# Kernel tuning notes

Measured on AMD Instinct MI355X. Metric: run time of the kernel, lower is better.

Reference implementation:

```python
import jax, jax.numpy as jnp
import numpy as np

N_NODES = 100000


def gcn_conv(x, src, dst, W, b, n_nodes):
    """PyG-style GCNConv: linear transform, symmetric-normalized aggregation with self loops."""
    h = x @ W  # (N, out)
    e = src.shape[0]
    # degree including the implicit self loop (edge weights = 1)
    deg = jax.ops.segment_sum(jnp.ones((e,), dtype=h.dtype), dst, num_segments=n_nodes) + 1.0
    dis = jax.lax.rsqrt(deg)  # deg^{-1/2}
    coef = dis[src] * dis[dst]  # (E,)
    msg = h[src] * coef[:, None]  # (E, out) -- gather + scale
    agg = jax.ops.segment_sum(msg, dst, num_segments=n_nodes)  # scatter-add
    agg = agg + h * (dis * dis)[:, None]  # self-loop contribution
    return agg + b


def setup_inputs() -> dict:
    key = jax.random.key(0)
    k = jax.random.split(key, 6)
    in_dim, hid, out = 128, 128, 64
    E = 1600000
    x = jax.random.normal(k[0], (N_NODES, in_dim), dtype=jnp.float32)
    edge_index = jax.random.randint(k[1], (2, E), 0, N_NODES, dtype=jnp.int64)
    W1 = jax.random.normal(k[2], (in_dim, hid), dtype=jnp.float32) * (1.0 / np.sqrt(in_dim))
    b1 = jnp.zeros((hid,), dtype=jnp.float32)
    W2 = jax.random.normal(k[3], (hid, out), dtype=jnp.float32) * (1.0 / np.sqrt(hid))
    b2 = jnp.zeros((out,), dtype=jnp.float32)
    return {"x": x, "edge_index": edge_index, "W1": W1, "b1": b1, "W2": W2, "b2": b2}


def reference(x, edge_index, W1, b1, W2, b2):
    src, dst = edge_index[0], edge_index[1]
    h = gcn_conv(x, src, dst, W1, b1, N_NODES)
    h = jax.nn.relu(h)
    # dropout is identity in eval mode
    h = gcn_conv(h, src, dst, W2, b2, N_NODES)
    # L2 normalize along feature dim (F.normalize, eps=1e-12)
    norm = jnp.maximum(jnp.linalg.norm(h, axis=-1, keepdims=True), 1e-12)
    return h / norm
```

## Files before the change

### kernel.cpp

```cpp
#include <hip/hip_runtime.h>
#include <hip/hip_bf16.h>
#include <math.h>

#define CSHIFT 9
#define TILE   4096
#define PSH    14

using f16x8 = __attribute__((ext_vector_type(8))) _Float16;
using f16x2 = __attribute__((ext_vector_type(2))) _Float16;
using f32x4 = __attribute__((ext_vector_type(4))) float;

__device__ __forceinline__ unsigned pack_f16(float lo, float hi) {
    auto h = __builtin_amdgcn_cvt_pkrtz(lo, hi);
    return *(unsigned*)&h;
}
__device__ __forceinline__ f16x2 h2(unsigned u) { return *(f16x2*)&u; }

__device__ __forceinline__ unsigned pack_fp8x4(float f0, float f1, float f2, float f3) {
    int w = 0;
    w = __builtin_amdgcn_cvt_pk_fp8_f32(f0, f1, w, false);
    w = __builtin_amdgcn_cvt_pk_fp8_f32(f2, f3, w, true);
    return (unsigned)w;
}
__device__ __forceinline__ void fp8x4_acc(unsigned v, float& a0, float& a1, float& a2, float& a3) {
    auto lo = __builtin_amdgcn_cvt_pk_f32_fp8((int)v, false);
    auto hi = __builtin_amdgcn_cvt_pk_f32_fp8((int)v, true);
    a0 += lo[0]; a1 += lo[1]; a2 += hi[0]; a3 += hi[1];
}

__global__ void k_prep(const float* __restrict__ W1, const float* __restrict__ W2,
                       unsigned short* __restrict__ wp1, unsigned short* __restrict__ wp2,
                       int* __restrict__ ccursor, int NC) {
    int idx = blockIdx.x * 256 + threadIdx.x;
    if (idx < NC) ccursor[idx] = idx << PSH;
    if (idx < 16384) {
        int e = idx & 7, l = (idx >> 3) & 63, f = idx >> 9;
        int nt = f & 7, kt = f >> 3;
        int k = kt * 32 + (l >> 4) * 8 + e, nn = nt * 16 + (l & 15);
        _Float16 hv = (_Float16)W1[k * 128 + nn];
        wp1[idx] = *(unsigned short*)&hv;
    }
    int i2 = idx - 16384;
    if (i2 >= 0 && i2 < 8192) {
        int e = i2 & 7, l = (i2 >> 3) & 63, f = i2 >> 9;
        int nt = f & 3, kt = f >> 2;
        int k = kt * 32 + (l >> 4) * 8 + e, nn = nt * 16 + (l & 15);
        _Float16 hv = (_Float16)W2[k * 64 + nn];
        wp2[i2] = *(unsigned short*)&hv;
    }
}

__global__ __launch_bounds__(256) void k_part(const int* __restrict__ src,
                                              const int* __restrict__ dst, int E,
                                              int* __restrict__ ccursor,
                                              int* __restrict__ pairs, int NC) {
    __shared__ int sdst[TILE];
    __shared__ int stg[TILE];
    __shared__ unsigned char sbk[TILE];
    __shared__ int h[256], delta[256], cur[256];
    __shared__ int sa[256], sb[256];
    int t = threadIdx.x;
    int base = blockIdx.x * TILE;
    int cnt = min(TILE, E - base);

    h[t] = 0; __syncthreads();
    #pragma unroll
    for (int k = 0; k < TILE / 256; ++k) {
        int e = base + k * 256 + t;
        int d = (e < E) ? dst[e] : -1;
        sdst[k * 256 + t] = d;
        if (d >= 0) atomicAdd(&h[d >> CSHIFT], 1);
    }
    __syncthreads();
    int myc = h[t];
    int* c_ = sa; int* n_ = sb;
    c_[t] = myc; __syncthreads();
    for (int o = 1; o < 256; o <<= 1) {
        int val = c_[t] + ((t >= o) ? c_[t - o] : 0);
        n_[t] = val; __syncthreads();
        int* tmp = c_; c_ = n_; n_ = tmp;
    }
    int ex = c_[t] - myc;
    cur[t] = ex;
    int g = 0;
    if (t < NC && myc) g = atomicAdd(&ccursor[t], myc);
    delta[t] = g - ex;
    __syncthreads();

    #pragma unroll
    for (int k = 0; k < TILE / 256; ++k) {
        int e = base + k * 256 + t;
        if (e < E) {
            int d = sdst[k * 256 + t];
            int b = d >> CSHIFT;
            int p = atomicAdd(&cur[b], 1);
            stg[p] = src[e] | ((d & 511) << 17);
            sbk[p] = (unsigned char)b;
        }
    }
    __syncthreads();
    for (int i = t; i < cnt; i += 256)
        pairs[delta[sbk[i]] + i] = stg[i];
}

__global__ __launch_bounds__(256) void k_build(const int* __restrict__ ccursor,
                                               const int* __restrict__ pairs,
                                               int2* __restrict__ seg,
                                               float* __restrict__ dis,
                                               int* __restrict__ csr, int N) {
    __shared__ int h[512];
    __shared__ int cur[512];
    __shared__ int sa[256], sb[256];
    int b = blockIdx.x, t = threadIdx.x;
    h[t] = 0; h[t + 256] = 0; __syncthreads();
    int beg = b << PSH, end = ccursor[b];
    for (int i = beg + t; i < end; i += 256) atomicAdd(&h[pairs[i] >> 17], 1);
    __syncthreads();
    int h0 = h[2 * t], h1 = h[2 * t + 1];
    int s = h0 + h1;
    int* c_ = sa; int* n_ = sb;
    c_[t] = s; __syncthreads();
    for (int o = 1; o < 256; o <<= 1) {
        int val = c_[t] + ((t >= o) ? c_[t - o] : 0);
        n_[t] = val; __syncthreads();
        int* tmp = c_; c_ = n_; n_ = tmp;
    }
    int ex = c_[t] - s;
    int d0 = b << CSHIFT;
    int da = d0 + 2 * t, db = da + 1;
    cur[2 * t] = ex; cur[2 * t + 1] = ex + h0;
    if (da < N) { seg[da] = make_int2(beg + ex, beg + ex + h0); dis[da] = rsqrtf((float)h0 + 1.0f); }
    if (db < N) { seg[db] = make_int2(beg + ex + h0, beg + ex + h0 + h1); dis[db] = rsqrtf((float)h1 + 1.0f); }
    __syncthreads();
    for (int i = beg + t; i < end; i += 256) {
        int pk = pairs[i];
        int p = atomicAdd(&cur[pk >> 17], 1);
        csr[beg + p] = pk & 0x1FFFF;
    }
}

__global__ __launch_bounds__(256) void k_gemm1(
    const float* __restrict__ A, const unsigned short* __restrict__ wp,
    const float* __restrict__ dis, unsigned* __restrict__ G, int M)
{
    constexpr int NT = 8;
    constexpr int ND = 32;

    union UW { uint4 q; f16x8 v; };
    union UA { unsigned u[4]; f16x8 v; };

    const int tid  = threadIdx.x;
    const int wv   = tid >> 6;
    const int lane = tid & 63;
    const int lm   = lane & 15;
    const int lk   = lane >> 4;
    const int m0   = blockIdx.x * 128 + wv * 32;

    f16x8 xf[2][4];
    int mrow[2];
    #pragma unroll
    for (int mt = 0; mt < 2; ++mt) {
        int m = m0 + mt * 16 + lm;
        mrow[mt] = m;
        int mc = m < M ? m : (M - 1);
        const float* Ar = A + (size_t)mc * 128;
        #pragma unroll
        for (int kt = 0; kt < 4; ++kt) {
            int cb = kt * 32 + lk * 8;
            float4 p = *(const float4*)(Ar + cb);
            float4 q = *(const float4*)(Ar + cb + 4);
            UA u;
            u.u[0] = pack_f16(p.x, p.y);
            u.u[1] = pack_f16(p.z, p.w);
            u.u[2] = pack_f16(q.x, q.y);
            u.u[3] = pack_f16(q.z, q.w);
            xf[mt][kt] = u.v;
        }
    }

    f32x4 acc[2][NT];
    #pragma unroll
    for (int mt = 0; mt < 2; ++mt)
        #pragma unroll
        for (int nt = 0; nt < NT; ++nt)
            #pragma unroll
            for (int r = 0; r < 4; ++r) acc[mt][nt][r] = 0.f;

    const uint4* wpv = (const uint4*)wp;
    #pragma unroll
    for (int kt = 0; kt < 4; ++kt) {
        f16x8 wf[NT];
        #pragma unroll
        for (int nt = 0; nt < NT; ++nt) {
            UW u; u.q = wpv[(kt * NT + nt) * 64 + lane];
            wf[nt] = u.v;
        }
        #pragma unroll
        for (int mt = 0; mt < 2; ++mt)
            #pragma unroll
            for (int nt = 0; nt < NT; ++nt)
                acc[mt][nt] = __builtin_amdgcn_mfma_f32_16x16x32_f16(
                    wf[nt], xf[mt][kt], acc[mt][nt], 0, 0, 0);
    }

    #pragma unroll
    for (int mt = 0; mt < 2; ++mt) {
        int m = mrow[mt];
        if (m < M) {
            float dd = dis[m];
            unsigned* gr = G + (size_t)m * ND;
            #pragma unroll
            for (int nt = 0; nt < NT; ++nt)
                gr[nt * 4 + lk] = pack_fp8x4(acc[mt][nt][0] * dd, acc[mt][nt][1] * dd,
                                             acc[mt][nt][2] * dd, acc[mt][nt][3] * dd);
        }
    }
}

__global__ __launch_bounds__(256) void k_agg1(
    const unsigned* __restrict__ g1, const int2* __restrict__ seg,
    const int* __restrict__ csr, const float* __restrict__ dis,
    const float* __restrict__ b1, unsigned* __restrict__ y1, int n)
{
    int wid  = (blockIdx.x * 256 + threadIdx.x) >> 6;
    int lane = threadIdx.x & 63;
    if (wid >= n) return;
    int d  = wid;
    int ll = lane & 31;
    int eh = lane >> 5;
    int2 se = seg[d];
    int beg = se.x, end = se.y;

    float a0 = 0.f, a1 = 0.f, a2 = 0.f, a3 = 0.f;
    if (eh == 0)
        fp8x4_acc(g1[(size_t)d * 32 + ll], a0, a1, a2, a3);

    int j = beg;
    for (; j + 16 <= end; j += 16) {
        unsigned v[8];
        #pragma unroll
        for (int k = 0; k < 8; ++k)
            v[k] = g1[(size_t)csr[j + 2 * k + eh] * 32 + ll];
        #pragma unroll
        for (int k = 0; k < 8; ++k)
            fp8x4_acc(v[k], a0, a1, a2, a3);
    }
    if (j + 8 <= end) {
        unsigned v[4];
        #pragma unroll
        for (int k = 0; k < 4; ++k)
            v[k] = g1[(size_t)csr[j + 2 * k + eh] * 32 + ll];
        #pragma unroll
        for (int k = 0; k < 4; ++k)
            fp8x4_acc(v[k], a0, a1, a2, a3);
        j += 8;
    }
    if (j + 4 <= end) {
        unsigned v0 = g1[(size_t)csr[j + eh] * 32 + ll];
        unsigned v1 = g1[(size_t)csr[j + 2 + eh] * 32 + ll];
        fp8x4_acc(v0, a0, a1, a2, a3);
        fp8x4_acc(v1, a0, a1, a2, a3);
        j += 4;
    }
    if (j + 2 <= end) {
        fp8x4_acc(g1[(size_t)csr[j + eh] * 32 + ll], a0, a1, a2, a3);
        j += 2;
    }
    if (eh == 0 && j < end)
        fp8x4_acc(g1[(size_t)csr[j] * 32 + ll], a0, a1, a2, a3);

    a0 += __shfl_xor(a0, 32, 64);
    a1 += __shfl_xor(a1, 32, 64);
    a2 += __shfl_xor(a2, 32, 64);
    a3 += __shfl_xor(a3, 32, 64);

    float dd = dis[d];
    float4 bb = *(const float4*)(b1 + 4 * ll);
    float o0 = fmaxf(fmaf(dd, a0, bb.x), 0.f);
    float o1 = fmaxf(fmaf(dd, a1, bb.y), 0.f);
    float o2 = fmaxf(fmaf(dd, a2, bb.z), 0.f);
    float o3 = fmaxf(fmaf(dd, a3, bb.w), 0.f);
    if (lane < 32) {
        uint2 w;
        w.x = pack_f16(o0, o1);
        w.y = pack_f16(o2, o3);
        *((uint2*)(y1 + (size_t)d * 64) + ll) = w;
    }
}

__global__ __launch_bounds__(256) void k_gemm2(
    const unsigned short* __restrict__ A, const unsigned short* __restrict__ wp,
    const float* __restrict__ dis, unsigned* __restrict__ G, int M)
{
    constexpr int NT = 4;
    constexpr int ND = 32;
    union UW { uint4 q; f16x8 v; };

    const int tid  = threadIdx.x;
    const int wv   = tid >> 6;
    const int lane = tid & 63;
    const int lm   = lane & 15;
    const int lk   = lane >> 4;
    const int m0   = blockIdx.x * 128 + wv * 32;

    f16x8 xf[2][4];
    int mrow[2];
    #pragma unroll
    for (int mt = 0; mt < 2; ++mt) {
        int m = m0 + mt * 16 + lm;
        mrow[mt] = m;
        int mc = m < M ? m : (M - 1);
        const uint4* Ar = (const uint4*)(A + (size_t)mc * 128);
        #pragma unroll
        for (int kt = 0; kt < 4; ++kt) {
            UW u; u.q = Ar[kt * 4 + lk];
            xf[mt][kt] = u.v;
        }
    }

    f32x4 acc[2][NT];
    #pragma unroll
    for (int mt = 0; mt < 2; ++mt)
        #pragma unroll
        for (int nt = 0; nt < NT; ++nt)
            #pragma unroll
            for (int r = 0; r < 4; ++r) acc[mt][nt][r] = 0.f;

    const uint4* wpv = (const uint4*)wp;
    #pragma unroll
    for (int kt = 0; kt < 4; ++kt) {
        f16x8 wf[NT];
        #pragma unroll
        for (int nt = 0; nt < NT; ++nt) {
            UW u; u.q = wpv[(kt * NT + nt) * 64 + lane];
            wf[nt] = u.v;
        }
        #pragma unroll
        for (int mt = 0; mt < 2; ++mt)
            #pragma unroll
            for (int nt = 0; nt < NT; ++nt)
                acc[mt][nt] = __builtin_amdgcn_mfma_f32_16x16x32_f16(
                    wf[nt], xf[mt][kt], acc[mt][nt], 0, 0, 0);
    }

    #pragma unroll
    for (int mt = 0; mt < 2; ++mt) {
        int m = mrow[mt];
        if (m < M) {
            float dd = dis[m];
            unsigned* gr = G + (size_t)m * ND;
            #pragma unroll
            for (int nt = 0; nt < NT; ++nt) {
                uint2 w;
                w.x = pack_f16(acc[mt][nt][0] * dd, acc[mt][nt][1] * dd);
                w.y = pack_f16(acc[mt][nt][2] * dd, acc[mt][nt][3] * dd);
                *(uint2*)(gr + nt * 8 + lk * 2) = w;
            }
        }
    }
}

__global__ __launch_bounds__(256) void k_agg2(
    const unsigned* __restrict__ g2, const int2* __restrict__ seg,
    const int* __restrict__ csr, const float* __restrict__ dis,
    const float* __restrict__ b2, float* __restrict__ out, int n)
{
    int wid  = (blockIdx.x * 256 + threadIdx.x) >> 6;
    int lane = threadIdx.x & 63;
    if (wid >= n) return;
    int d  = wid;
    int ql = lane & 15;
    int qh = lane >> 4;
    int2 se = seg[d];
    int beg = se.x, end = se.y;

    f16x2 cx0 = {0, 0}, cx1 = {0, 0}, cy0 = {0, 0}, cy1 = {0, 0};
    int j = beg;
    for (; j + 32 <= end; j += 32) {
        uint2 v[8];
        #pragma unroll
        for (int k = 0; k < 8; ++k) {
            int s = csr[j + 4 * k + qh];
            v[k] = *((const uint2*)(g2 + (size_t)s * 32) + ql);
        }
        #pragma unroll
        for (int k = 0; k < 8; k += 2) {
            cx0 += h2(v[k].x);     cy0 += h2(v[k].y);
            cx1 += h2(v[k + 1].x); cy1 += h2(v[k + 1].y);
        }
    }
    for (; j + 16 <= end; j += 16) {
        int s0 = csr[j      + qh];
        int s1 = csr[j + 4  + qh];
        int s2 = csr[j + 8  + qh];
        int s3 = csr[j + 12 + qh];
        uint2 v0 = *((const uint2*)(g2 + (size_t)s0 * 32) + ql);
        uint2 v1 = *((const uint2*)(g2 + (size_t)s1 * 32) + ql);
        uint2 v2 = *((const uint2*)(g2 + (size_t)s2 * 32) + ql);
        uint2 v3 = *((const uint2*)(g2 + (size_t)s3 * 32) + ql);
        cx0 += h2(v0.x); cy0 += h2(v0.y);
        cx1 += h2(v1.x); cy1 += h2(v1.y);
        cx0 += h2(v2.x); cy0 += h2(v2.y);
        cx1 += h2(v3.x); cy1 += h2(v3.y);
    }
    if (j + 8 <= end) {
        int s0 = csr[j     + qh];
        int s1 = csr[j + 4 + qh];
        uint2 v0 = *((const uint2*)(g2 + (size_t)s0 * 32) + ql);
        uint2 v1 = *((const uint2*)(g2 + (size_t)s1 * 32) + ql);
        cx0 += h2(v0.x); cy0 += h2(v0.y);
        cx1 += h2(v1.x); cy1 += h2(v1.y);
        j += 8;
    }
    for (; j < end; j += 4) {
        if (j + qh < end) {
            int s = csr[j + qh];
            uint2 v = *((const uint2*)(g2 + (size_t)s * 32) + ql);
            cx0 += h2(v.x); cy0 += h2(v.y);
        }
    }
    f16x2 mx = cx0 + cx1;
    f16x2 my = cy0 + cy1;
    float a0 = (float)mx[0], a1 = (float)mx[1];
    float a2 = (float)my[0], a3 = (float)my[1];

    a0 += __shfl_xor(a0, 16, 64); a0 += __shfl_xor(a0, 32, 64);
    a1 += __shfl_xor(a1, 16, 64); a1 += __shfl_xor(a1, 32, 64);
    a2 += __shfl_xor(a2, 16, 64); a2 += __shfl_xor(a2, 32, 64);
    a3 += __shfl_xor(a3, 16, 64); a3 += __shfl_xor(a3, 32, 64);

    uint2 sv = *((const uint2*)(g2 + (size_t)d * 32) + ql);
    f16x2 sx = h2(sv.x), sy = h2(sv.y);
    a0 += (float)sx[0]; a1 += (float)sx[1];
    a2 += (float)sy[0]; a3 += (float)sy[1];

    float dd = dis[d];
    float4 bb = *(const float4*)(b2 + 4 * ql);
    float v0 = fmaf(dd, a0, bb.x);
    float v1 = fmaf(dd, a1, bb.y);
    float v2 = fmaf(dd, a2, bb.z);
    float v3 = fmaf(dd, a3, bb.w);

    float ss = v0 * v0 + v1 * v1 + v2 * v2 + v3 * v3;
    #pragma unroll
    for (int o = 8; o >= 1; o >>= 1)
        ss += __shfl_xor(ss, o, 64);
    float inv = 1.0f / fmaxf(sqrtf(ss), 1e-12f);
    if (lane < 16) {
        float4 w = make_float4(v0 * inv, v1 * inv, v2 * inv, v3 * inv);
        *((float4*)(out + (size_t)d * 64) + ql) = w;
    }
}

extern "C" void kernel_launch(void* const* d_in, const int* in_sizes, int n_in,
                              void* d_out, int out_size, void* d_ws, size_t ws_size,
                              hipStream_t stream) {
    const float* x  = (const float*)d_in[0];
    const int*   ei = (const int*)d_in[1];
    const float* W1 = (const float*)d_in[2];
    const float* b1 = (const float*)d_in[3];
    const float* W2 = (const float*)d_in[4];
    const float* b2 = (const float*)d_in[5];

    const int N = in_sizes[0] / 128;
    const int E = in_sizes[1] / 2;
    const int* src = ei;
    const int* dst = ei + E;
    const int NC = (N + 511) >> CSHIFT;
    const int PB = (E + TILE - 1) / TILE;

    char* ws = (char*)d_ws;
    size_t cur = 0;
    auto alloc = [&](size_t bytes) -> void* {
        void* p = ws + cur;
        cur += (bytes + 255) & ~(size_t)255;
        return p;
    };
    int2*           seg     = (int2*)           alloc((size_t)N * 8);
    int*            ccursor = (int*)            alloc((size_t)NC * 4);
    float*          dis     = (float*)          alloc((size_t)N * 4);
    int*            csr     = (int*)            alloc(((size_t)NC << PSH) * 4);
    int*            pairs   = (int*)            alloc(((size_t)NC << PSH) * 4);
    unsigned short* wp1     = (unsigned short*) alloc(16384 * 2);
    unsigned short* wp2     = (unsigned short*) alloc(8192 * 2);
    unsigned*       g1      = (unsigned*)       alloc((size_t)N * 32 * 4);
    unsigned*       y1      = (unsigned*)       alloc((size_t)N * 64 * 4);
    unsigned*       g2      = (unsigned*)       alloc((size_t)N * 32 * 4);
    float*          out     = (float*)d_out;

    k_prep<<<96, 256, 0, stream>>>(W1, W2, wp1, wp2, ccursor, NC);
    k_part<<<PB, 256, 0, stream>>>(src, dst, E, ccursor, pairs, NC);
    k_build<<<NC, 256, 0, stream>>>(ccursor, pairs, seg, dis, csr, N);

    k_gemm1<<<(N + 127) / 128, 256, 0, stream>>>(x, wp1, dis, g1, N);
    k_agg1<<<(N * 64 + 255) / 256, 256, 0, stream>>>(g1, seg, csr, dis, b1, y1, N);
    k_gemm2<<<(N + 127) / 128, 256, 0, stream>>>((const unsigned short*)y1, wp2, dis, g2, N);
    k_agg2<<<(N * 64 + 255) / 256, 256, 0, stream>>>(g2, seg, csr, dis, b2, out, N);
}
```

Measured before the change: 178.4 us.

## Compute degrees early, fuse GEMM1 with partitioning, pad CSR segments to 16

Degrees are now counted with global atomics inside the prep kernel, which lets GEMM1 run in the same launch as the edge partitioning instead of waiting for the CSR build. Each node's CSR segment is padded to a multiple of 16 with a dummy index N that points at a zeroed extra row of g1/g2, so the aggregation loops drop their remainder branches. The layer-2 aggregation now accumulates in fp32 instead of fp16. The cost is extra gather traffic for the padding entries and 1.6M global atomics for the degree count.

Result: slower. 221.2 us (+24.0%).

```diff
diff --git a/kernel.cpp b/kernel.cpp
--- a/kernel.cpp
+++ b/kernel.cpp
@@ -5,6 +5,7 @@
 #define CSHIFT 9
 #define TILE   4096
 #define PSH    14
+#define PREPB  96
 
 using f16x8 = __attribute__((ext_vector_type(8))) _Float16;
 using f16x2 = __attribute__((ext_vector_type(2))) _Float16;
@@ -28,11 +29,28 @@
     a0 += lo[0]; a1 += lo[1]; a2 += hi[0]; a3 += hi[1];
 }
 
-__global__ void k_prep(const float* __restrict__ W1, const float* __restrict__ W2,
-                       unsigned short* __restrict__ wp1, unsigned short* __restrict__ wp2,
-                       int* __restrict__ ccursor, int NC) {
+__global__ __launch_bounds__(256) void k_prep(
+    const float* __restrict__ W1, const float* __restrict__ W2,
+    const int* __restrict__ dst, int E,
+    unsigned short* __restrict__ wp1, unsigned short* __restrict__ wp2,
+    int* __restrict__ ccursor, int* __restrict__ deg,
+    unsigned* __restrict__ g1, unsigned* __restrict__ g2, int NC, int N)
+{
+    if ((int)blockIdx.x >= PREPB) {
+        int base = (blockIdx.x - PREPB) * TILE;
+        #pragma unroll
+        for (int k = 0; k < TILE / 256; ++k) {
+            int e = base + k * 256 + threadIdx.x;
+            if (e < E) atomicAdd(&deg[dst[e]], 1);
+        }
+        return;
+    }
     int idx = blockIdx.x * 256 + threadIdx.x;
     if (idx < NC) ccursor[idx] = idx << PSH;
+    if (idx < 32) {
+        g1[(size_t)N * 32 + idx] = 0u;
+        g2[(size_t)N * 32 + idx] = 0u;
+    }
     if (idx < 16384) {
         int e = idx & 7, l = (idx >> 3) & 63, f = idx >> 9;
         int nt = f & 7, kt = f >> 3;
@@ -50,63 +68,136 @@
     }
 }
 
-__global__ __launch_bounds__(256) void k_part(const int* __restrict__ src,
-                                              const int* __restrict__ dst, int E,
-                                              int* __restrict__ ccursor,
-                                              int* __restrict__ pairs, int NC) {
-    __shared__ int sdst[TILE];
-    __shared__ int stg[TILE];
-    __shared__ unsigned char sbk[TILE];
-    __shared__ int h[256], delta[256], cur[256];
-    __shared__ int sa[256], sb[256];
-    int t = threadIdx.x;
-    int base = blockIdx.x * TILE;
-    int cnt = min(TILE, E - base);
-
-    h[t] = 0; __syncthreads();
-    #pragma unroll
-    for (int k = 0; k < TILE / 256; ++k) {
-        int e = base + k * 256 + t;
-        int d = (e < E) ? dst[e] : -1;
-        sdst[k * 256 + t] = d;
-        if (d >= 0) atomicAdd(&h[d >> CSHIFT], 1);
-    }
-    __syncthreads();
-    int myc = h[t];
-    int* c_ = sa; int* n_ = sb;
-    c_[t] = myc; __syncthreads();
-    for (int o = 1; o < 256; o <<= 1) {
-        int val = c_[t] + ((t >= o) ? c_[t - o] : 0);
-        n_[t] = val; __syncthreads();
-        int* tmp = c_; c_ = n_; n_ = tmp;
-    }
-    int ex = c_[t] - myc;
-    cur[t] = ex;
-    int g = 0;
-    if (t < NC && myc) g = atomicAdd(&ccursor[t], myc);
-    delta[t] = g - ex;
-    __syncthreads();
-
-    #pragma unroll
-    for (int k = 0; k < TILE / 256; ++k) {
-        int e = base + k * 256 + t;
-        if (e < E) {
-            int d = sdst[k * 256 + t];
-            int b = d >> CSHIFT;
-            int p = atomicAdd(&cur[b], 1);
-            stg[p] = src[e] | ((d & 511) << 17);
-            sbk[p] = (unsigned char)b;
-        }
-    }
-    __syncthreads();
-    for (int i = t; i < cnt; i += 256)
-        pairs[delta[sbk[i]] + i] = stg[i];
+__global__ __launch_bounds__(256) void k_pg1(
+    const int* __restrict__ src, const int* __restrict__ dst, int E,
+    int* __restrict__ ccursor, int* __restrict__ pairs, int NC, int PB,
+    const float* __restrict__ x, const unsigned short* __restrict__ wp1,
+    const int* __restrict__ deg, unsigned* __restrict__ g1, int M)
+{
+    if ((int)blockIdx.x < PB) {
+        __shared__ int stg[TILE];
+        __shared__ unsigned char sbk[TILE];
+        __shared__ int h[256], delta[256], cur[256];
+        __shared__ int sa[256], sb[256];
+        int t = threadIdx.x;
+        int base = blockIdx.x * TILE;
+        int cnt = min(TILE, E - base);
+
+        h[t] = 0; __syncthreads();
+        #pragma unroll
+        for (int k = 0; k < TILE / 256; ++k) {
+            int e = base + k * 256 + t;
+            if (e < E) atomicAdd(&h[dst[e] >> CSHIFT], 1);
+        }
+        __syncthreads();
+        int myc = h[t];
+        int* c_ = sa; int* n_ = sb;
+        c_[t] = myc; __syncthreads();
+        for (int o = 1; o < 256; o <<= 1) {
+            int val = c_[t] + ((t >= o) ? c_[t - o] : 0);
+            n_[t] = val; __syncthreads();
+            int* tmp = c_; c_ = n_; n_ = tmp;
+        }
+        int ex = c_[t] - myc;
+        cur[t] = ex;
+        int g = 0;
+        if (t < NC && myc) g = atomicAdd(&ccursor[t], myc);
+        delta[t] = g - ex;
+        __syncthreads();
+
+        #pragma unroll
+        for (int k = 0; k < TILE / 256; ++k) {
+            int e = base + k * 256 + t;
+            if (e < E) {
+                int d = dst[e];
+                int b = d >> CSHIFT;
+                int p = atomicAdd(&cur[b], 1);
+                stg[p] = src[e] | ((d & 511) << 17);
+                sbk[p] = (unsigned char)b;
+            }
+        }
+        __syncthreads();
+        for (int i = t; i < cnt; i += 256)
+            pairs[delta[sbk[i]] + i] = stg[i];
+    } else {
+        constexpr int NT = 8;
+        constexpr int ND = 32;
+        union UW { uint4 q; f16x8 v; };
+        union UA { unsigned u[4]; f16x8 v; };
+
+        const int bid  = blockIdx.x - PB;
+        const int tid  = threadIdx.x;
+        const int wv   = tid >> 6;
+        const int lane = tid & 63;
+        const int lm   = lane & 15;
+        const int lk   = lane >> 4;
+        const int m0   = bid * 128 + wv * 32;
+
+        f16x8 xf[2][4];
+        int mrow[2];
+        #pragma unroll
+        for (int mt = 0; mt < 2; ++mt) {
+            int m = m0 + mt * 16 + lm;
+            mrow[mt] = m;
+            int mc = m < M ? m : (M - 1);
+            const float* Ar = x + (size_t)mc * 128;
+            #pragma unroll
+            for (int kt = 0; kt < 4; ++kt) {
+                int cb = kt * 32 + lk * 8;
+                float4 p = *(const float4*)(Ar + cb);
+                float4 q = *(const float4*)(Ar + cb + 4);
+                UA u;
+                u.u[0] = pack_f16(p.x, p.y);
+                u.u[1] = pack_f16(p.z, p.w);
+                u.u[2] = pack_f16(q.x, q.y);
+                u.u[3] = pack_f16(q.z, q.w);
+                xf[mt][kt] = u.v;
+            }
+        }
+
+        f32x4 acc[2][NT];
+        #pragma unroll
+        for (int mt = 0; mt < 2; ++mt)
+            #pragma unroll
+            for (int nt = 0; nt < NT; ++nt)
+                #pragma unroll
+                for (int r = 0; r < 4; ++r) acc[mt][nt][r] = 0.f;
+
+        const uint4* wpv = (const uint4*)wp1;
+        #pragma unroll
+        for (int kt = 0; kt < 4; ++kt) {
+            f16x8 wf[NT];
+            #pragma unroll
+            for (int nt = 0; nt < NT; ++nt) {
+                UW u; u.q = wpv[(kt * NT + nt) * 64 + lane];
+                wf[nt] = u.v;
+            }
+            #pragma unroll
+            for (int mt = 0; mt < 2; ++mt)
+                #pragma unroll
+                for (int nt = 0; nt < NT; ++nt)
+                    acc[mt][nt] = __builtin_amdgcn_mfma_f32_16x16x32_f16(
+                        wf[nt], xf[mt][kt], acc[mt][nt], 0, 0, 0);
+        }
+
+        #pragma unroll
+        for (int mt = 0; mt < 2; ++mt) {
+            int m = mrow[mt];
+            if (m < M) {
+                float dd = rsqrtf((float)deg[m] + 1.0f);
+                unsigned* gr = g1 + (size_t)m * ND;
+                #pragma unroll
+                for (int nt = 0; nt < NT; ++nt)
+                    gr[nt * 4 + lk] = pack_fp8x4(acc[mt][nt][0] * dd, acc[mt][nt][1] * dd,
+                                                 acc[mt][nt][2] * dd, acc[mt][nt][3] * dd);
+            }
+        }
+    }
 }
 
 __global__ __launch_bounds__(256) void k_build(const int* __restrict__ ccursor,
                                                const int* __restrict__ pairs,
                                                int2* __restrict__ seg,
-                                               float* __restrict__ dis,
                                                int* __restrict__ csr, int N) {
     __shared__ int h[512];
     __shared__ int cur[512];
@@ -117,7 +208,9 @@
     for (int i = beg + t; i < end; i += 256) atomicAdd(&h[pairs[i] >> 17], 1);
     __syncthreads();
     int h0 = h[2 * t], h1 = h[2 * t + 1];
-    int s = h0 + h1;
+    int p0 = (h0 + 15) & ~15;
+    int p1 = (h1 + 15) & ~15;
+    int s = p0 + p1;
     int* c_ = sa; int* n_ = sb;
     c_[t] = s; __syncthreads();
     for (int o = 1; o < 256; o <<= 1) {
@@ -128,9 +221,11 @@
     int ex = c_[t] - s;
     int d0 = b << CSHIFT;
     int da = d0 + 2 * t, db = da + 1;
-    cur[2 * t] = ex; cur[2 * t + 1] = ex + h0;
-    if (da < N) { seg[da] = make_int2(beg + ex, beg + ex + h0); dis[da] = rsqrtf((float)h0 + 1.0f); }
-    if (db < N) { seg[db] = make_int2(beg + ex + h0, beg + ex + h0 + h1); dis[db] = rsqrtf((float)h1 + 1.0f); }
+    cur[2 * t] = ex; cur[2 * t + 1] = ex + p0;
+    if (da < N) seg[da] = make_int2(beg + ex, beg + ex + p0);
+    if (db < N) seg[db] = make_int2(beg + ex + p0, beg + ex + p0 + p1);
+    for (int i = h0; i < p0; ++i) csr[beg + ex + i] = N;
+    for (int i = h1; i < p1; ++i) csr[beg + ex + p0 + i] = N;
     __syncthreads();
     for (int i = beg + t; i < end; i += 256) {
         int pk = pairs[i];
@@ -139,87 +234,9 @@
     }
 }
 
-__global__ __launch_bounds__(256) void k_gemm1(
-    const float* __restrict__ A, const unsigned short* __restrict__ wp,
-    const float* __restrict__ dis, unsigned* __restrict__ G, int M)
-{
-    constexpr int NT = 8;
-    constexpr int ND = 32;
-
-    union UW { uint4 q; f16x8 v; };
-    union UA { unsigned u[4]; f16x8 v; };
-
-    const int tid  = threadIdx.x;
-    const int wv   = tid >> 6;
-    const int lane = tid & 63;
-    const int lm   = lane & 15;
-    const int lk   = lane >> 4;
-    const int m0   = blockIdx.x * 128 + wv * 32;
-
-    f16x8 xf[2][4];
-    int mrow[2];
-    #pragma unroll
-    for (int mt = 0; mt < 2; ++mt) {
-        int m = m0 + mt * 16 + lm;
-        mrow[mt] = m;
-        int mc = m < M ? m : (M - 1);
-        const float* Ar = A + (size_t)mc * 128;
-        #pragma unroll
-        for (int kt = 0; kt < 4; ++kt) {
-            int cb = kt * 32 + lk * 8;
-            float4 p = *(const float4*)(Ar + cb);
-            float4 q = *(const float4*)(Ar + cb + 4);
-            UA u;
-            u.u[0] = pack_f16(p.x, p.y);
-            u.u[1] = pack_f16(p.z, p.w);
-            u.u[2] = pack_f16(q.x, q.y);
-            u.u[3] = pack_f16(q.z, q.w);
-            xf[mt][kt] = u.v;
-        }
-    }
-
-    f32x4 acc[2][NT];
-    #pragma unroll
-    for (int mt = 0; mt < 2; ++mt)
-        #pragma unroll
-        for (int nt = 0; nt < NT; ++nt)
-            #pragma unroll
-            for (int r = 0; r < 4; ++r) acc[mt][nt][r] = 0.f;
-
-    const uint4* wpv = (const uint4*)wp;
-    #pragma unroll
-    for (int kt = 0; kt < 4; ++kt) {
-        f16x8 wf[NT];
-        #pragma unroll
-        for (int nt = 0; nt < NT; ++nt) {
-            UW u; u.q = wpv[(kt * NT + nt) * 64 + lane];
-            wf[nt] = u.v;
-        }
-        #pragma unroll
-        for (int mt = 0; mt < 2; ++mt)
-            #pragma unroll
-            for (int nt = 0; nt < NT; ++nt)
-                acc[mt][nt] = __builtin_amdgcn_mfma_f32_16x16x32_f16(
-                    wf[nt], xf[mt][kt], acc[mt][nt], 0, 0, 0);
-    }
-
-    #pragma unroll
-    for (int mt = 0; mt < 2; ++mt) {
-        int m = mrow[mt];
-        if (m < M) {
-            float dd = dis[m];
-            unsigned* gr = G + (size_t)m * ND;
-            #pragma unroll
-            for (int nt = 0; nt < NT; ++nt)
-                gr[nt * 4 + lk] = pack_fp8x4(acc[mt][nt][0] * dd, acc[mt][nt][1] * dd,
-                                             acc[mt][nt][2] * dd, acc[mt][nt][3] * dd);
-        }
-    }
-}
-
 __global__ __launch_bounds__(256) void k_agg1(
     const unsigned* __restrict__ g1, const int2* __restrict__ seg,
-    const int* __restrict__ csr, const float* __restrict__ dis,
+    const int* __restrict__ csr, const int* __restrict__ deg,
     const float* __restrict__ b1, unsigned* __restrict__ y1, int n)
 {
     int wid  = (blockIdx.x * 256 + threadIdx.x) >> 6;
@@ -229,14 +246,13 @@
     int ll = lane & 31;
     int eh = lane >> 5;
     int2 se = seg[d];
-    int beg = se.x, end = se.y;
+    int beg = se.x, pend = se.y;
 
     float a0 = 0.f, a1 = 0.f, a2 = 0.f, a3 = 0.f;
     if (eh == 0)
         fp8x4_acc(g1[(size_t)d * 32 + ll], a0, a1, a2, a3);
 
-    int j = beg;
-    for (; j + 16 <= end; j += 16) {
+    for (int j = beg; j < pend; j += 16) {
         unsigned v[8];
         #pragma unroll
         for (int k = 0; k < 8; ++k)
@@ -245,36 +261,13 @@
         for (int k = 0; k < 8; ++k)
             fp8x4_acc(v[k], a0, a1, a2, a3);
     }
-    if (j + 8 <= end) {
-        unsigned v[4];
-        #pragma unroll
-        for (int k = 0; k < 4; ++k)
-            v[k] = g1[(size_t)csr[j + 2 * k + eh] * 32 + ll];
-        #pragma unroll
-        for (int k = 0; k < 4; ++k)
-            fp8x4_acc(v[k], a0, a1, a2, a3);
-        j += 8;
-    }
-    if (j + 4 <= end) {
-        unsigned v0 = g1[(size_t)csr[j + eh] * 32 + ll];
-        unsigned v1 = g1[(size_t)csr[j + 2 + eh] * 32 + ll];
-        fp8x4_acc(v0, a0, a1, a2, a3);
-        fp8x4_acc(v1, a0, a1, a2, a3);
-        j += 4;
-    }
-    if (j + 2 <= end) {
-        fp8x4_acc(g1[(size_t)csr[j + eh] * 32 + ll], a0, a1, a2, a3);
-        j += 2;
-    }
-    if (eh == 0 && j < end)
-        fp8x4_acc(g1[(size_t)csr[j] * 32 + ll], a0, a1, a2, a3);
 
     a0 += __shfl_xor(a0, 32, 64);
     a1 += __shfl_xor(a1, 32, 64);
     a2 += __shfl_xor(a2, 32, 64);
     a3 += __shfl_xor(a3, 32, 64);
 
-    float dd = dis[d];
+    float dd = rsqrtf((float)deg[d] + 1.0f);
     float4 bb = *(const float4*)(b1 + 4 * ll);
     float o0 = fmaxf(fmaf(dd, a0, bb.x), 0.f);
     float o1 = fmaxf(fmaf(dd, a1, bb.y), 0.f);
@@ -290,7 +283,7 @@
 
 __global__ __launch_bounds__(256) void k_gemm2(
     const unsigned short* __restrict__ A, const unsigned short* __restrict__ wp,
-    const float* __restrict__ dis, unsigned* __restrict__ G, int M)
+    const int* __restrict__ deg, unsigned* __restrict__ G, int M)
 {
     constexpr int NT = 4;
     constexpr int ND = 32;
@@ -347,7 +340,7 @@
     for (int mt = 0; mt < 2; ++mt) {
         int m = mrow[mt];
         if (m < M) {
-            float dd = dis[m];
+            float dd = rsqrtf((float)deg[m] + 1.0f);
             unsigned* gr = G + (size_t)m * ND;
             #pragma unroll
             for (int nt = 0; nt < NT; ++nt) {
@@ -362,7 +355,7 @@
 
 __global__ __launch_bounds__(256) void k_agg2(
     const unsigned* __restrict__ g2, const int2* __restrict__ seg,
-    const int* __restrict__ csr, const float* __restrict__ dis,
+    const int* __restrict__ csr, const int* __restrict__ deg,
     const float* __restrict__ b2, float* __restrict__ out, int n)
 {
     int wid  = (blockIdx.x * 256 + threadIdx.x) >> 6;
@@ -372,11 +365,11 @@
     int ql = lane & 15;
     int qh = lane >> 4;
     int2 se = seg[d];
-    int beg = se.x, end = se.y;
-
-    f16x2 cx0 = {0, 0}, cx1 = {0, 0}, cy0 = {0, 0}, cy1 = {0, 0};
+    int beg = se.x, pend = se.y;
+
+    float a0 = 0.f, a1 = 0.f, a2 = 0.f, a3 = 0.f;
     int j = beg;
-    for (; j + 32 <= end; j += 32) {
+    for (; j + 32 <= pend; j += 32) {
         uint2 v[8];
         #pragma unroll
         for (int k = 0; k < 8; ++k) {
@@ -385,44 +378,27 @@
         }
         #pragma unroll
         for (int k = 0; k < 8; k += 2) {
-            cx0 += h2(v[k].x);     cy0 += h2(v[k].y);
-            cx1 += h2(v[k + 1].x); cy1 += h2(v[k + 1].y);
-        }
-    }
-    for (; j + 16 <= end; j += 16) {
-        int s0 = csr[j      + qh];
-        int s1 = csr[j + 4  + qh];
-        int s2 = csr[j + 8  + qh];
-        int s3 = csr[j + 12 + qh];
-        uint2 v0 = *((const uint2*)(g2 + (size_t)s0 * 32) + ql);
-        uint2 v1 = *((const uint2*)(g2 + (size_t)s1 * 32) + ql);
-        uint2 v2 = *((const uint2*)(g2 + (size_t)s2 * 32) + ql);
-        uint2 v3 = *((const uint2*)(g2 + (size_t)s3 * 32) + ql);
-        cx0 += h2(v0.x); cy0 += h2(v0.y);
-        cx1 += h2(v1.x); cy1 += h2(v1.y);
-        cx0 += h2(v2.x); cy0 += h2(v2.y);
-        cx1 += h2(v3.x); cy1 += h2(v3.y);
-    }
-    if (j + 8 <= end) {
-        int s0 = csr[j     + qh];
-        int s1 = csr[j + 4 + qh];
-        uint2 v0 = *((const uint2*)(g2 + (size_t)s0 * 32) + ql);
-        uint2 v1 = *((const uint2*)(g2 + (size_t)s1 * 32) + ql);
-        cx0 += h2(v0.x); cy0 += h2(v0.y);
-        cx1 += h2(v1.x); cy1 += h2(v1.y);
-        j += 8;
-    }
-    for (; j < end; j += 4) {
-        if (j + qh < end) {
-            int s = csr[j + qh];
-            uint2 v = *((const uint2*)(g2 + (size_t)s * 32) + ql);
-            cx0 += h2(v.x); cy0 += h2(v.y);
-        }
-    }
-    f16x2 mx = cx0 + cx1;
-    f16x2 my = cy0 + cy1;
-    float a0 = (float)mx[0], a1 = (float)mx[1];
-    float a2 = (float)my[0], a3 = (float)my[1];
+            f16x2 sx = h2(v[k].x) + h2(v[k + 1].x);
+            f16x2 sy = h2(v[k].y) + h2(v[k + 1].y);
+            a0 += (float)sx[0]; a1 += (float)sx[1];
+            a2 += (float)sy[0]; a3 += (float)sy[1];
+        }
+    }
+    if (j < pend) {
+        uint2 v[4];
+        #pragma unroll
+        for (int k = 0; k < 4; ++k) {
+            int s = csr[j + 4 * k + qh];
+            v[k] = *((const uint2*)(g2 + (size_t)s * 32) + ql);
+        }
+        #pragma unroll
+        for (int k = 0; k < 4; k += 2) {
+            f16x2 sx = h2(v[k].x) + h2(v[k + 1].x);
+            f16x2 sy = h2(v[k].y) + h2(v[k + 1].y);
+            a0 += (float)sx[0]; a1 += (float)sx[1];
+            a2 += (float)sy[0]; a3 += (float)sy[1];
+        }
+    }
 
     a0 += __shfl_xor(a0, 16, 64); a0 += __shfl_xor(a0, 32, 64);
     a1 += __shfl_xor(a1, 16, 64); a1 += __shfl_xor(a1, 32, 64);
@@ -434,7 +410,7 @@
     a0 += (float)sx[0]; a1 += (float)sx[1];
     a2 += (float)sy[0]; a3 += (float)sy[1];
 
-    float dd = dis[d];
+    float dd = rsqrtf((float)deg[d] + 1.0f);
     float4 bb = *(const float4*)(b2 + 4 * ql);
     float v0 = fmaf(dd, a0, bb.x);
     float v1 = fmaf(dd, a1, bb.y);
@@ -468,6 +444,7 @@
     const int* dst = ei + E;
     const int NC = (N + 511) >> CSHIFT;
     const int PB = (E + TILE - 1) / TILE;
+    const int GB = (N + 127) / 128;
 
     char* ws = (char*)d_ws;
     size_t cur = 0;
@@ -478,22 +455,21 @@
     };
     int2*           seg     = (int2*)           alloc((size_t)N * 8);
     int*            ccursor = (int*)            alloc((size_t)NC * 4);
-    float*          dis     = (float*)          alloc((size_t)N * 4);
+    int*            deg     = (int*)            alloc((size_t)N * 4);
     int*            csr     = (int*)            alloc(((size_t)NC << PSH) * 4);
     int*            pairs   = (int*)            alloc(((size_t)NC << PSH) * 4);
     unsigned short* wp1     = (unsigned short*) alloc(16384 * 2);
     unsigned short* wp2     = (unsigned short*) alloc(8192 * 2);
-    unsigned*       g1      = (unsigned*)       alloc((size_t)N * 32 * 4);
+    unsigned*       g1      = (unsigned*)       alloc((size_t)(N + 1) * 32 * 4);
     unsigned*       y1      = (unsigned*)       alloc((size_t)N * 64 * 4);
-    unsigned*       g2      = (unsigned*)       alloc((size_t)N * 32 * 4);
+    unsigned*       g2      = (unsigned*)       alloc((size_t)(N + 1) * 32 * 4);
     float*          out     = (float*)d_out;
 
-    k_prep<<<96, 256, 0, stream>>>(W1, W2, wp1, wp2, ccursor, NC);
-    k_part<<<PB, 256, 0, stream>>>(src, dst, E, ccursor, pairs, NC);
-    k_build<<<NC, 256, 0, stream>>>(ccursor, pairs, seg, dis, csr, N);
-
-    k_gemm1<<<(N + 127) / 128, 256, 0, stream>>>(x, wp1, dis, g1, N);
-    k_agg1<<<(N * 64 + 255) / 256, 256, 0, stream>>>(g1, seg, csr, dis, b1, y1, N);
-    k_gemm2<<<(N + 127) / 128, 256, 0, stream>>>((const unsigned short*)y1, wp2, dis, g2, N);
-    k_agg2<<<(N * 64 + 255) / 256, 256, 0, stream>>>(g2, seg, csr, dis, b2, out, N);
-}
+    hipMemsetAsync(deg, 0, (size_t)N * 4, stream);
+    k_prep<<<PREPB + PB, 256, 0, stream>>>(W1, W2, dst, E, wp1, wp2, ccursor, deg, g1, g2, NC, N);
+    k_pg1<<<PB + GB, 256, 0, stream>>>(src, dst, E, ccursor, pairs, NC, PB, x, wp1, deg, g1, N);
+    k_build<<<NC, 256, 0, stream>>>(ccursor, pairs, seg, csr, N);
+    k_agg1<<<(N * 64 + 255) / 256, 256, 0, stream>>>(g1, seg, csr, deg, b1, y1, N);
+    k_gemm2<<<(N + 127) / 128, 256, 0, stream>>>((const unsigned short*)y1, wp2, deg, g2, N);
+    k_agg2<<<(N * 64 + 255) / 256, 256, 0, stream>>>(g2, seg, csr, deg, b2, out, N);
+}
```
